# Kernel optimization log

Measured on AMD Instinct MI355X. Metric: run time of the kernel, lower is better.

Reference implementation:

```python
import jax, jax.numpy as jnp
import numpy as np

VMF_KAPPA = 30.0      # vMF concentration
THRESHOLD = 0.0       # vc_thresholds
OCC_LIKELY = 0.6      # occ_likely[0]
NUM_MIXTURES = 4
EPS_L1 = 1e-12        # torch F.normalize eps


def _l1_normalize(x, axis):
    n = jnp.sum(jnp.abs(x), axis=axis, keepdims=True)
    return x / jnp.maximum(n, EPS_L1)


def _crop_or_pad(mm, H, W):
    # center crop or zero-pad mix model spatial dims to (H, W); shapes are static
    _, _, hm, wm = mm.shape
    if hm < H:
        d1 = (H - hm) // 2
        mm = jnp.pad(mm, ((0, 0), (0, 0), (d1, H - hm - d1), (0, 0)))
    elif hm > H:
        d1 = (hm - H) // 2
        mm = mm[:, :, d1:d1 + H, :]
    if wm < W:
        d1 = (W - wm) // 2
        mm = jnp.pad(mm, ((0, 0), (0, 0), (0, 0), (d1, W - wm - d1)))
    elif wm > W:
        d1 = (wm - W) // 2
        mm = mm[:, :, :, d1:d1 + W]
    return mm


def setup_inputs() -> dict:
    key = jax.random.key(0)
    k1, k2, k3, k4 = jax.random.split(key, 4)
    B, C, H, W = 32, 512, 56, 56
    VC = 512              # number of vMF codebook vectors
    KM = 48               # num_classes(12) * num_mixtures(4)
    NCLUT = 5             # clutter models
    return {
        "vgg_feat": jax.random.normal(k1, (B, C, H, W), dtype=jnp.float32),
        "conv_weight": jax.random.normal(k2, (VC, C, 1, 1), dtype=jnp.float32),
        "mix_model": jax.random.uniform(k3, (KM, VC, H, W), dtype=jnp.float32),
        "clutter_model": jax.random.uniform(k4, (NCLUT, VC), dtype=jnp.float32),
    }


def reference(vgg_feat, conv_weight, mix_model, clutter_model):
    B, C, H, W = vgg_feat.shape
    # --- Conv1o1: cosine similarity between L2-normalized features and codebook ---
    xnorm = jnp.linalg.norm(vgg_feat, axis=1, keepdims=True)
    xnorm = xnorm + (xnorm == 0).astype(vgg_feat.dtype)  # avoid div-by-zero
    xn = vgg_feat / xnorm
    w = conv_weight[:, :, 0, 0]                           # (vc, C) 1x1 kernel
    wn = w / jnp.linalg.norm(w, axis=1, keepdims=True)
    cos = jnp.einsum('bchw,kc->bkhw', xn, wn)             # (B, vc, H, W)
    # --- vMF activation ---
    act = jnp.exp(VMF_KAPPA * cos) * (cos > THRESHOLD).astype(cos.dtype)
    # --- PointwiseInferenceLayer (vmf, use_mixture_bg=True) ---
    ck = _l1_normalize(jnp.clip(clutter_model, 0.0, 1.0), axis=1)  # (N, vc)
    bg = jnp.einsum('bkhw,nk->bnhw', act, ck)                      # (B, N, H, W)
    background = jnp.log(bg * OCC_LIKELY + 1e-10)
    background = jnp.max(background, axis=1, keepdims=True)        # (B, 1, H, W)
    background = background[:, None, None]                         # (B,1,1,1,H,W)

    mm = _l1_normalize(jnp.clip(mix_model, 0.0, 1.0), axis=1)      # (KM, vc, Hm, Wm)
    mm = _crop_or_pad(mm, H, W)
    fg = jnp.einsum('bkhw,mkhw->bmhw', act, mm)                    # (B, KM, H, W)
    foreground = jnp.log(fg * (1.0 - OCC_LIKELY) + 1e-10)
    num_classes = mm.shape[0] // NUM_MIXTURES
    foreground = foreground.reshape(B, num_classes, NUM_MIXTURES, 1, H, W)
    per_model = jnp.maximum(foreground, background).sum(axis=(-1, -2))  # (B,K,M,1)
    scores = per_model.max(axis=-1).max(axis=-1)                        # (B, K)
    mix_likeli = scores / (H * W)
    # SoftMaxTemp(2.0)
    z = jnp.exp(jnp.clip(mix_likeli * 2.0, -88.7, 88.7))
    soft = z / jnp.sum(z, axis=1, keepdims=True)
    return soft, vgg_feat, mix_likeli
```

## Files before the change

kernel.cpp:

```cpp
#include <hip/hip_runtime.h>

#define B_ 32
#define C_ 512
#define HW_ 3136
#define KF_ 512
#define KM_ 48
#define NCL_ 5

typedef __attribute__((ext_vector_type(8))) short short8;
typedef __attribute__((ext_vector_type(4))) short short4v;
typedef __attribute__((ext_vector_type(4))) float floatx4;
typedef unsigned int u32;
typedef u32 __attribute__((address_space(1))) gu32;
typedef u32 __attribute__((address_space(3))) lu32;

__device__ __forceinline__ unsigned short f2bf(float f) {
    union { float f; unsigned u; } v; v.f = f;
    unsigned r = v.u + 0x7FFFu + ((v.u >> 16) & 1u);
    return (unsigned short)(r >> 16);
}
__device__ __forceinline__ float bf2f(unsigned short u) {
    union { unsigned u; float f; } v; v.u = ((unsigned)u) << 16;
    return v.f;
}
__device__ __forceinline__ void gl2lds16(const unsigned short* g, unsigned short* l) {
    __builtin_amdgcn_global_load_lds((const gu32*)g, (lu32*)l, 16, 0, 0);
}

__global__ __launch_bounds__(64) void prep_kernel(const float* __restrict__ w,
                                                  const float* __restrict__ cl,
                                                  unsigned short* __restrict__ wn,
                                                  float* __restrict__ ck) {
    int bid = blockIdx.x, t = threadIdx.x;
    if (bid < KF_) {
        const float* row = w + (size_t)bid * C_;
        float ss = 0.f;
        float x[8];
#pragma unroll
        for (int j = 0; j < 8; ++j) { x[j] = row[t * 8 + j]; ss += x[j] * x[j]; }
        for (int m = 32; m >= 1; m >>= 1) ss += __shfl_xor(ss, m);
        float inv = 1.f / sqrtf(ss);
#pragma unroll
        for (int j = 0; j < 8; ++j) wn[(size_t)bid * C_ + t * 8 + j] = f2bf(x[j] * inv);
    } else {
        int n = bid - KF_;
        if (n >= NCL_) return;
        const float* row = cl + (size_t)n * KF_;
        float s = 0.f;
        float v[8];
#pragma unroll
        for (int j = 0; j < 8; ++j) {
            float x = row[t * 8 + j];
            x = fminf(fmaxf(x, 0.f), 1.f);
            v[j] = x; s += x;
        }
        for (int m = 32; m >= 1; m >>= 1) s += __shfl_xor(s, m);
        float inv = 1.f / fmaxf(s, 1e-12f);
#pragma unroll
        for (int j = 0; j < 8; ++j) ck[(size_t)n * KF_ + t * 8 + j] = v[j] * inv;
    }
}

__global__ __launch_bounds__(512) void xprep_kernel(const float* __restrict__ vgg,
                                                    unsigned short* __restrict__ xnt,
                                                    float* __restrict__ invn,
                                                    float* __restrict__ out_vgg,
                                                    int write_vgg) {
    int pt = blockIdx.x, b = blockIdx.y;
    int tid = threadIdx.x;
    int px = tid & 63, cq = tid >> 6;
    __shared__ __align__(16) unsigned short tile[64][512];
    __shared__ float ssp[8][64];
    const float* vcol = vgg + (size_t)b * C_ * HW_ + pt * 64 + px;
    float* ovcol = out_vgg + (size_t)b * C_ * HW_ + pt * 64 + px;

    float ss = 0.f;
#pragma unroll
    for (int j = 0; j < 16; ++j) {
        int c0 = cq * 64 + j * 4;
        float x0 = vcol[(size_t)(c0 + 0) * HW_];
        float x1 = vcol[(size_t)(c0 + 1) * HW_];
        float x2 = vcol[(size_t)(c0 + 2) * HW_];
        float x3 = vcol[(size_t)(c0 + 3) * HW_];
        ss += x0 * x0 + x1 * x1 + x2 * x2 + x3 * x3;
        short4v pk;
        pk[0] = (short)f2bf(x0); pk[1] = (short)f2bf(x1);
        pk[2] = (short)f2bf(x2); pk[3] = (short)f2bf(x3);
        *(short4v*)&tile[px][c0] = pk;
        if (write_vgg) {
            ovcol[(size_t)(c0 + 0) * HW_] = x0;
            ovcol[(size_t)(c0 + 1) * HW_] = x1;
            ovcol[(size_t)(c0 + 2) * HW_] = x2;
            ovcol[(size_t)(c0 + 3) * HW_] = x3;
        }
    }
    ssp[cq][px] = ss;
    __syncthreads();
    if (tid < 64) {
        float s = 0.f;
#pragma unroll
        for (int q = 0; q < 8; ++q) s += ssp[q][tid];
        float n = sqrtf(s);
        invn[(size_t)b * HW_ + pt * 64 + tid] = (n == 0.f) ? 1.f : 1.f / n;
    }
    __syncthreads();
    int row = tid >> 3, ch = tid & 7;
    unsigned short* orow = xnt + ((size_t)b * HW_ + pt * 64 + row) * 512;
#pragma unroll
    for (int j = 0; j < 8; ++j) {
        int c8 = (ch + 8 * j) * 8;
        *(short8*)(orow + c8) = *(const short8*)&tile[row][c8];
    }
}

__global__ __launch_bounds__(256) void gemm_act_kernel(const unsigned short* __restrict__ xnt,
                                                       const unsigned short* __restrict__ wn,
                                                       const float* __restrict__ invn,
                                                       const float* __restrict__ ck,
                                                       unsigned short* __restrict__ act,
                                                       float* __restrict__ bgacc) {
    int pt = blockIdx.x, ft = blockIdx.y;
    int tid = threadIdx.x, lane = tid & 63, w = tid >> 6;
    int wm = w & 1, wq = w >> 1;
    __shared__ __align__(16) unsigned short a_lds[128 * 64];
    __shared__ __align__(16) unsigned short b_lds[128 * 64];
    __shared__ float ck_l[NCL_ * KF_];
    __shared__ float inv_l[128];
    __shared__ float bga_l[128 * NCL_];

    for (int i = tid; i < NCL_ * KF_; i += 256) ck_l[i] = ck[i];
    if (tid < 128) inv_l[tid] = invn[(size_t)pt * 128 + tid];
    for (int i = tid; i < 128 * NCL_; i += 256) bga_l[i] = 0.f;

    const unsigned short* ga = wn + ((size_t)(ft * 128) + (tid >> 3)) * 512 + (tid & 7) * 8;
    const unsigned short* gb = xnt + ((size_t)pt * 128 + (tid >> 3)) * 512 + (tid & 7) * 8;
    unsigned short* la = a_lds + (tid >> 3) * 64 + (tid & 7) * 8;
    unsigned short* lb = b_lds + (tid >> 3) * 64 + (tid & 7) * 8;

    floatx4 acc[4][4] = {};
    for (int ks = 0; ks < 8; ++ks) {
#pragma unroll
        for (int s = 0; s < 4; ++s) {
            gl2lds16(ga + (size_t)s * 32 * 512 + ks * 64, la + s * 32 * 64);
            gl2lds16(gb + (size_t)s * 32 * 512 + ks * 64, lb + s * 32 * 64);
        }
        __syncthreads();
#pragma unroll
        for (int k2 = 0; k2 < 2; ++k2) {
            short8 af[4], bf[4];
#pragma unroll
            for (int i = 0; i < 4; ++i) {
                af[i] = *(const short8*)&a_lds[(wm * 64 + i * 16 + (lane & 15)) * 64 + k2 * 32 + (lane >> 4) * 8];
                bf[i] = *(const short8*)&b_lds[(wq * 64 + i * 16 + (lane & 15)) * 64 + k2 * 32 + (lane >> 4) * 8];
            }
#pragma unroll
            for (int mi = 0; mi < 4; ++mi)
#pragma unroll
                for (int ni = 0; ni < 4; ++ni)
                    acc[mi][ni] = __builtin_amdgcn_mfma_f32_16x16x32_bf16(af[mi], bf[ni], acc[mi][ni], 0, 0, 0);
        }
        __syncthreads();
    }

#pragma unroll
    for (int ni = 0; ni < 4; ++ni) {
        int px_l = wq * 64 + ni * 16 + (lane & 15);
        float inv = inv_l[px_l];
        size_t row_g = (size_t)pt * 128 + px_l;
        float bp[NCL_] = {0.f, 0.f, 0.f, 0.f, 0.f};
#pragma unroll
        for (int mi = 0; mi < 4; ++mi) {
            int f_g = ft * 128 + wm * 64 + mi * 16 + (lane >> 4) * 4;
            short4v pk;
            float av[4];
#pragma unroll
            for (int r = 0; r < 4; ++r) {
                float cv = acc[mi][ni][r] * inv;
                float a = cv > 0.f ? __expf(30.f * cv) : 0.f;
                av[r] = a;
                pk[r] = (short)f2bf(a);
            }
            *(short4v*)(act + row_g * 512 + f_g) = pk;
#pragma unroll
            for (int n = 0; n < NCL_; ++n)
                bp[n] += av[0] * ck_l[n * KF_ + f_g] + av[1] * ck_l[n * KF_ + f_g + 1] +
                         av[2] * ck_l[n * KF_ + f_g + 2] + av[3] * ck_l[n * KF_ + f_g + 3];
        }
#pragma unroll
        for (int n = 0; n < NCL_; ++n) {
            float v = bp[n];
            v += __shfl_xor(v, 16);
            v += __shfl_xor(v, 32);
            if ((lane >> 4) == 0) atomicAdd(&bga_l[px_l * NCL_ + n], v);
        }
    }
    __syncthreads();
    if (tid < 128) {
        size_t row_g = (size_t)pt * 128 + tid;
#pragma unroll
        for (int n = 0; n < NCL_; ++n)
            atomicAdd(&bgacc[row_g * 8 + n], bga_l[tid * NCL_ + n]);
    }
}

__global__ __launch_bounds__(512, 4) void fg_kernel(const unsigned short* __restrict__ act,
                                                    const float* __restrict__ mm,
                                                    const float* __restrict__ bgacc,
                                                    float* __restrict__ pm) {
    int p0 = blockIdx.x * 16;
    int mt = blockIdx.y;
    int tid = threadIdx.x;
    int lane = tid & 63, wid = tid >> 6;

    __shared__ __align__(16) unsigned short actl[4 * 4224];
    __shared__ __align__(16) unsigned short mml[4 * 2176];
    __shared__ float csum_s[16 * 16];
    __shared__ float pms[16 * 32];
    __shared__ float bgs[32 * 16];

    if (tid < 256) csum_s[tid] = 0.f;
    pms[tid] = 0.f;
    {
        int bb = tid >> 4, pp = tid & 15;
        const float* bga = bgacc + ((size_t)bb * HW_ + p0 + pp) * 8;
        float mx = -1e30f;
#pragma unroll
        for (int n = 0; n < NCL_; ++n) mx = fmaxf(mx, logf(bga[n] * 0.6f + 1e-10f));
        bgs[tid] = mx;
    }

    int akg = tid & 3, ap = (tid >> 2) & 15, ab0 = tid >> 6;
    int mmm = tid >> 5, mkq = (tid >> 2) & 7, mpq = tid & 3;
    const float* mbase = mm + ((size_t)(mt * 16 + mmm) * KF_ + mkq * 4) * HW_ + p0 + mpq * 4;

    const short8* fA[2];
    const short8* fB[2][2];
#pragma unroll
    for (int e = 0; e < 2; ++e) {
        int pp = wid * 2 + e;
        fA[e] = (const short8*)&mml[(lane >> 4) * 2176 + pp * 136 + (lane & 15) * 8];
#pragma unroll
        for (int bf = 0; bf < 2; ++bf)
            fB[e][bf] = (const short8*)&actl[(lane >> 4) * 4224 + pp * 264 + (bf * 16 + (lane & 15)) * 8];
    }

    floatx4 acc[2][2] = {};
    float csr[4] = {};

    short8 areg[4];
    floatx4 mreg[4];
#pragma unroll
    for (int j = 0; j < 4; ++j)
        areg[j] = *(const short8*)(act + ((size_t)(ab0 + j * 8) * HW_ + p0 + ap) * KF_ + akg * 8);
#pragma unroll
    for (int kk = 0; kk < 4; ++kk)
        mreg[kk] = *(const floatx4*)(mbase + (size_t)kk * HW_);

    for (int ch = 0; ch < 16; ++ch) {
        __syncthreads();
#pragma unroll
        for (int j = 0; j < 4; ++j)
            *(short8*)&actl[akg * 4224 + ap * 264 + (ab0 + j * 8) * 8] = areg[j];
#pragma unroll
        for (int i = 0; i < 4; ++i) {
            float c0 = fminf(fmaxf(mreg[0][i], 0.f), 1.f);
            float c1 = fminf(fmaxf(mreg[1][i], 0.f), 1.f);
            float c2 = fminf(fmaxf(mreg[2][i], 0.f), 1.f);
            float c3 = fminf(fmaxf(mreg[3][i], 0.f), 1.f);
            csr[i] += c0 + c1 + c2 + c3;
            short4v pk;
            pk[0] = (short)f2bf(c0); pk[1] = (short)f2bf(c1);
            pk[2] = (short)f2bf(c2); pk[3] = (short)f2bf(c3);
            *(short4v*)&mml[(mkq >> 1) * 2176 + (mpq * 4 + i) * 136 + mmm * 8 + (mkq & 1) * 4] = pk;
        }
        if (ch < 15) {
            int k0 = (ch + 1) * 32;
#pragma unroll
            for (int j = 0; j < 4; ++j)
                areg[j] = *(const short8*)(act + ((size_t)(ab0 + j * 8) * HW_ + p0 + ap) * KF_ + k0 + akg * 8);
#pragma unroll
            for (int kk = 0; kk < 4; ++kk)
                mreg[kk] = *(const floatx4*)(mbase + (size_t)(k0 + kk) * HW_);
        }
        __syncthreads();
#pragma unroll
        for (int e = 0; e < 2; ++e) {
            short8 af = *fA[e];
            short8 b0 = *fB[e][0];
            short8 b1 = *fB[e][1];
            acc[e][0] = __builtin_amdgcn_mfma_f32_16x16x32_bf16(af, b0, acc[e][0], 0, 0, 0);
            acc[e][1] = __builtin_amdgcn_mfma_f32_16x16x32_bf16(af, b1, acc[e][1], 0, 0, 0);
        }
    }

#pragma unroll
    for (int i = 0; i < 4; ++i)
        atomicAdd(&csum_s[mmm * 16 + mpq * 4 + i], csr[i]);
    __syncthreads();

#pragma unroll
    for (int e = 0; e < 2; ++e) {
        int pp = wid * 2 + e;
#pragma unroll
        for (int bf = 0; bf < 2; ++bf) {
            int bcol = bf * 16 + (lane & 15);
            float bgv = bgs[bcol * 16 + pp];
#pragma unroll
            for (int r = 0; r < 4; ++r) {
                int m = (lane >> 4) * 4 + r;
                float invn = 1.f / fmaxf(csum_s[m * 16 + pp], 1e-12f);
                float v = fmaxf(logf(acc[e][bf][r] * invn * 0.4f + 1e-10f), bgv);
                atomicAdd(&pms[m * 32 + bcol], v);
            }
        }
    }
    __syncthreads();
    {
        int m = tid >> 5, bcol = tid & 31;
        atomicAdd(&pm[(size_t)bcol * KM_ + mt * 16 + m], pms[m * 32 + bcol]);
    }
}

__global__ __launch_bounds__(64) void final_kernel(const float* __restrict__ pm,
                                                   float* __restrict__ out_soft,
                                                   float* __restrict__ out_ml) {
    int b = threadIdx.x;
    if (b >= B_) return;
    float ml[12];
#pragma unroll
    for (int c = 0; c < 12; ++c) {
        float s = -1e30f;
#pragma unroll
        for (int j = 0; j < 4; ++j) s = fmaxf(s, pm[(size_t)b * KM_ + c * 4 + j]);
        ml[c] = s / (float)HW_;
    }
    float z[12], zs = 0.f;
#pragma unroll
    for (int c = 0; c < 12; ++c) {
        float e = fminf(fmaxf(ml[c] * 2.f, -88.7f), 88.7f);
        z[c] = expf(e); zs += z[c];
    }
#pragma unroll
    for (int c = 0; c < 12; ++c) {
        out_soft[(size_t)b * 12 + c] = z[c] / zs;
        out_ml[(size_t)b * 12 + c] = ml[c];
    }
}

extern "C" void kernel_launch(void* const* d_in, const int* in_sizes, int n_in,
                              void* d_out, int out_size, void* d_ws, size_t ws_size,
                              hipStream_t stream) {
    const float* vgg = (const float*)d_in[0];
    const float* cw  = (const float*)d_in[1];
    const float* mmp = (const float*)d_in[2];
    const float* cl  = (const float*)d_in[3];
    float* out = (float*)d_out;
    char* ws = (char*)d_ws;

    unsigned short* wn   = (unsigned short*)(ws);
    float* ck            = (float*)(ws + 524288);
    float* invn          = (float*)(ws + 534528);
    float* pm            = (float*)(ws + 935936);
    float* bgacc         = (float*)(ws + 942080);
    unsigned short* xnt  = (unsigned short*)(ws + 4153344);
    const size_t ACT_OFF = 4153344 + 102760448;
    const size_t ACT_BYTES = (size_t)B_ * HW_ * KF_ * 2;

    int big_ws = (ws_size >= ACT_OFF + ACT_BYTES) ? 1 : 0;
    unsigned short* act = big_ws ? (unsigned short*)(ws + ACT_OFF)
                                 : (unsigned short*)(out + 384);

    hipMemsetAsync(pm, 0, (size_t)B_ * KM_ * sizeof(float), stream);
    hipMemsetAsync(bgacc, 0, (size_t)B_ * HW_ * 8 * sizeof(float), stream);
    prep_kernel<<<dim3(KF_ + NCL_), dim3(64), 0, stream>>>(cw, cl, wn, ck);
    xprep_kernel<<<dim3(49, 32), dim3(512), 0, stream>>>(vgg, xnt, invn, out + 384, big_ws);
    gemm_act_kernel<<<dim3(784, 4), dim3(256), 0, stream>>>(xnt, wn, invn, ck, act, bgacc);
    fg_kernel<<<dim3(196, 3), dim3(512), 0, stream>>>(act, mmp, bgacc, pm);
    final_kernel<<<1, 64, 0, stream>>>(pm, out, out + 384 + (size_t)B_ * C_ * HW_);
    if (!big_ws)
        hipMemcpyAsync(out + 384, vgg, (size_t)B_ * C_ * HW_ * sizeof(float),
                       hipMemcpyDeviceToDevice, stream);
}
```

Measured before the change: 496.4 us.

## Chunk act layout by K and process all 48 mixtures per fg block

The act tensor is now written in a K-chunked layout (16 chunks of 32 features, pixel-major within each chunk), so each fg block reads a contiguous 64-byte run per pixel per chunk. fg_kernel drops the 3-way mixture split in the grid and has each block compute all 48 mixtures for its 16 pixels, so act is read once from global memory instead of three times. The cost is a larger per-thread register footprint (48 prefetched mix-model floats plus 12 accumulators), more shared memory, and only 196 blocks, which may leave the GPU's compute units underfilled.

```diff
diff --git a/kernel.cpp b/kernel.cpp
--- a/kernel.cpp
+++ b/kernel.cpp
@@ -171,6 +171,8 @@
 #pragma unroll
         for (int mi = 0; mi < 4; ++mi) {
             int f_g = ft * 128 + wm * 64 + mi * 16 + (lane >> 4) * 4;
+            int chn = ft * 4 + wm * 2 + (mi >> 1);
+            int kin = (mi & 1) * 16 + (lane >> 4) * 4;
             short4v pk;
             float av[4];
 #pragma unroll
@@ -180,7 +182,7 @@
                 av[r] = a;
                 pk[r] = (short)f2bf(a);
             }
-            *(short4v*)(act + row_g * 512 + f_g) = pk;
+            *(short4v*)(act + ((size_t)chn * 100352 + row_g) * 32 + kin) = pk;
 #pragma unroll
             for (int n = 0; n < NCL_; ++n)
                 bp[n] += av[0] * ck_l[n * KF_ + f_g] + av[1] * ck_l[n * KF_ + f_g + 1] +
@@ -203,121 +205,149 @@
     }
 }
 
-__global__ __launch_bounds__(512, 4) void fg_kernel(const unsigned short* __restrict__ act,
-                                                    const float* __restrict__ mm,
-                                                    const float* __restrict__ bgacc,
-                                                    float* __restrict__ pm) {
+__global__ __launch_bounds__(512) void fg_kernel(const unsigned short* __restrict__ act,
+                                                 const float* __restrict__ mm,
+                                                 const float* __restrict__ bgacc,
+                                                 float* __restrict__ pm) {
     int p0 = blockIdx.x * 16;
-    int mt = blockIdx.y;
     int tid = threadIdx.x;
     int lane = tid & 63, wid = tid >> 6;
-
-    __shared__ __align__(16) unsigned short actl[4 * 4224];
-    __shared__ __align__(16) unsigned short mml[4 * 2176];
-    __shared__ float csum_s[16 * 16];
-    __shared__ float pms[16 * 32];
-    __shared__ float bgs[32 * 16];
-
-    if (tid < 256) csum_s[tid] = 0.f;
-    pms[tid] = 0.f;
+    int li = lane & 15, q = lane >> 4;
+
+    __shared__ __align__(16) unsigned short actl[16 * 1154];
+    __shared__ __align__(16) unsigned short mml[16 * 1730];
+    __shared__ float csum_s[768];
+    __shared__ float pms[1536];
+    __shared__ float bgs[512];
+
+    for (int i = tid; i < 768; i += 512) csum_s[i] = 0.f;
+    for (int i = tid; i < 1536; i += 512) pms[i] = 0.f;
     {
-        int bb = tid >> 4, pp = tid & 15;
-        const float* bga = bgacc + ((size_t)bb * HW_ + p0 + pp) * 8;
+        int b = tid >> 4, px = tid & 15;
+        const float* bga = bgacc + ((size_t)b * HW_ + p0 + px) * 8;
         float mx = -1e30f;
 #pragma unroll
         for (int n = 0; n < NCL_; ++n) mx = fmaxf(mx, logf(bga[n] * 0.6f + 1e-10f));
         bgs[tid] = mx;
     }
 
-    int akg = tid & 3, ap = (tid >> 2) & 15, ab0 = tid >> 6;
-    int mmm = tid >> 5, mkq = (tid >> 2) & 7, mpq = tid & 3;
-    const float* mbase = mm + ((size_t)(mt * 16 + mmm) * KF_ + mkq * 4) * HW_ + p0 + mpq * 4;
-
-    const short8* fA[2];
-    const short8* fB[2][2];
+    int sb = tid >> 4, spx = tid & 15;
+    int m1 = sb;
+    int m2 = 32 + (sb & 15);
+    int kqo = (tid >> 8) * 4;
+
+    const unsigned short* ap = act + ((size_t)sb * HW_ + p0 + spx) * 32;
+    const float* mp1 = mm + (size_t)m1 * KF_ * HW_ + p0 + spx;
+    const float* mp2 = mm + ((size_t)m2 * KF_ + kqo * 4) * HW_ + p0 + spx;
+
+    unsigned short* awr = &actl[spx * 1154 + sb * 36];
+    unsigned short* mwr1 = &mml[spx * 1730 + m1 * 36];
+    unsigned short* mwr2 = &mml[spx * 1730 + m2 * 36];
+
+    float csum1 = 0.f, csum2 = 0.f;
+    short8 areg[4];
+    float m1r[32], m2r[16];
+    floatx4 acc[2][3][2] = {};
+
+#pragma unroll
+    for (int j = 0; j < 4; ++j) areg[j] = *(const short8*)(ap + j * 8);
+#pragma unroll
+    for (int kq = 0; kq < 8; ++kq)
+#pragma unroll
+        for (int kk = 0; kk < 4; ++kk)
+            m1r[kq * 4 + kk] = mp1[(size_t)(kq * 4 + kk) * HW_];
+#pragma unroll
+    for (int jj = 0; jj < 4; ++jj)
+#pragma unroll
+        for (int kk = 0; kk < 4; ++kk)
+            m2r[jj * 4 + kk] = mp2[(size_t)(jj * 4 + kk) * HW_];
+
+#pragma unroll 1
+    for (int ch = 0; ch < 16; ++ch) {
+        __syncthreads();
+#pragma unroll
+        for (int j = 0; j < 4; ++j) *(short8*)(awr + j * 8) = areg[j];
+#pragma unroll
+        for (int kq = 0; kq < 8; ++kq) {
+            short4v pk;
+#pragma unroll
+            for (int kk = 0; kk < 4; ++kk) {
+                float x = fminf(fmaxf(m1r[kq * 4 + kk], 0.f), 1.f);
+                csum1 += x;
+                pk[kk] = (short)f2bf(x);
+            }
+            *(short4v*)(mwr1 + kq * 4) = pk;
+        }
+#pragma unroll
+        for (int jj = 0; jj < 4; ++jj) {
+            short4v pk;
+#pragma unroll
+            for (int kk = 0; kk < 4; ++kk) {
+                float x = fminf(fmaxf(m2r[jj * 4 + kk], 0.f), 1.f);
+                csum2 += x;
+                pk[kk] = (short)f2bf(x);
+            }
+            *(short4v*)(mwr2 + (kqo + jj) * 4) = pk;
+        }
+        __syncthreads();
+        if (ch < 15) {
+            ap += (size_t)100352 * 32;
+            mp1 += (size_t)32 * HW_;
+            mp2 += (size_t)32 * HW_;
+#pragma unroll
+            for (int j = 0; j < 4; ++j) areg[j] = *(const short8*)(ap + j * 8);
+#pragma unroll
+            for (int kq = 0; kq < 8; ++kq)
+#pragma unroll
+                for (int kk = 0; kk < 4; ++kk)
+                    m1r[kq * 4 + kk] = mp1[(size_t)(kq * 4 + kk) * HW_];
+#pragma unroll
+            for (int jj = 0; jj < 4; ++jj)
+#pragma unroll
+                for (int kk = 0; kk < 4; ++kk)
+                    m2r[jj * 4 + kk] = mp2[(size_t)(jj * 4 + kk) * HW_];
+        }
+#pragma unroll
+        for (int e = 0; e < 2; ++e) {
+            int pp = wid * 2 + e;
+            short8 bfr0 = *(const short8*)&actl[pp * 1154 + li * 36 + q * 8];
+            short8 bfr1 = *(const short8*)&actl[pp * 1154 + (16 + li) * 36 + q * 8];
+#pragma unroll
+            for (int mf = 0; mf < 3; ++mf) {
+                short8 af = *(const short8*)&mml[pp * 1730 + (mf * 16 + li) * 36 + q * 8];
+                acc[e][mf][0] = __builtin_amdgcn_mfma_f32_16x16x32_bf16(af, bfr0, acc[e][mf][0], 0, 0, 0);
+                acc[e][mf][1] = __builtin_amdgcn_mfma_f32_16x16x32_bf16(af, bfr1, acc[e][mf][1], 0, 0, 0);
+            }
+        }
+    }
+
+    csum_s[m1 * 16 + spx] = csum1;
+    atomicAdd(&csum_s[m2 * 16 + spx], csum2);
+    __syncthreads();
+
 #pragma unroll
     for (int e = 0; e < 2; ++e) {
         int pp = wid * 2 + e;
-        fA[e] = (const short8*)&mml[(lane >> 4) * 2176 + pp * 136 + (lane & 15) * 8];
-#pragma unroll
-        for (int bf = 0; bf < 2; ++bf)
-            fB[e][bf] = (const short8*)&actl[(lane >> 4) * 4224 + pp * 264 + (bf * 16 + (lane & 15)) * 8];
-    }
-
-    floatx4 acc[2][2] = {};
-    float csr[4] = {};
-
-    short8 areg[4];
-    floatx4 mreg[4];
-#pragma unroll
-    for (int j = 0; j < 4; ++j)
-        areg[j] = *(const short8*)(act + ((size_t)(ab0 + j * 8) * HW_ + p0 + ap) * KF_ + akg * 8);
-#pragma unroll
-    for (int kk = 0; kk < 4; ++kk)
-        mreg[kk] = *(const floatx4*)(mbase + (size_t)kk * HW_);
-
-    for (int ch = 0; ch < 16; ++ch) {
-        __syncthreads();
-#pragma unroll
-        for (int j = 0; j < 4; ++j)
-            *(short8*)&actl[akg * 4224 + ap * 264 + (ab0 + j * 8) * 8] = areg[j];
-#pragma unroll
-        for (int i = 0; i < 4; ++i) {
-            float c0 = fminf(fmaxf(mreg[0][i], 0.f), 1.f);
-            float c1 = fminf(fmaxf(mreg[1][i], 0.f), 1.f);
-            float c2 = fminf(fmaxf(mreg[2][i], 0.f), 1.f);
-            float c3 = fminf(fmaxf(mreg[3][i], 0.f), 1.f);
-            csr[i] += c0 + c1 + c2 + c3;
-            short4v pk;
-            pk[0] = (short)f2bf(c0); pk[1] = (short)f2bf(c1);
-            pk[2] = (short)f2bf(c2); pk[3] = (short)f2bf(c3);
-            *(short4v*)&mml[(mkq >> 1) * 2176 + (mpq * 4 + i) * 136 + mmm * 8 + (mkq & 1) * 4] = pk;
-        }
-        if (ch < 15) {
-            int k0 = (ch + 1) * 32;
-#pragma unroll
-            for (int j = 0; j < 4; ++j)
-                areg[j] = *(const short8*)(act + ((size_t)(ab0 + j * 8) * HW_ + p0 + ap) * KF_ + k0 + akg * 8);
-#pragma unroll
-            for (int kk = 0; kk < 4; ++kk)
-                mreg[kk] = *(const floatx4*)(mbase + (size_t)(k0 + kk) * HW_);
-        }
-        __syncthreads();
-#pragma unroll
-        for (int e = 0; e < 2; ++e) {
-            short8 af = *fA[e];
-            short8 b0 = *fB[e][0];
-            short8 b1 = *fB[e][1];
-            acc[e][0] = __builtin_amdgcn_mfma_f32_16x16x32_bf16(af, b0, acc[e][0], 0, 0, 0);
-            acc[e][1] = __builtin_amdgcn_mfma_f32_16x16x32_bf16(af, b1, acc[e][1], 0, 0, 0);
-        }
-    }
-
-#pragma unroll
-    for (int i = 0; i < 4; ++i)
-        atomicAdd(&csum_s[mmm * 16 + mpq * 4 + i], csr[i]);
+#pragma unroll
+        for (int bf = 0; bf < 2; ++bf) {
+            int b = bf * 16 + li;
+            float bgv = bgs[b * 16 + pp];
+#pragma unroll
+            for (int mf = 0; mf < 3; ++mf) {
+#pragma unroll
+                for (int r = 0; r < 4; ++r) {
+                    int m = mf * 16 + q * 4 + r;
+                    float inv = 1.f / fmaxf(csum_s[m * 16 + pp], 1e-12f);
+                    float v = fmaxf(logf(acc[e][mf][bf][r] * inv * 0.4f + 1e-10f), bgv);
+                    atomicAdd(&pms[m * 32 + b], v);
+                }
+            }
+        }
+    }
     __syncthreads();
-
-#pragma unroll
-    for (int e = 0; e < 2; ++e) {
-        int pp = wid * 2 + e;
-#pragma unroll
-        for (int bf = 0; bf < 2; ++bf) {
-            int bcol = bf * 16 + (lane & 15);
-            float bgv = bgs[bcol * 16 + pp];
-#pragma unroll
-            for (int r = 0; r < 4; ++r) {
-                int m = (lane >> 4) * 4 + r;
-                float invn = 1.f / fmaxf(csum_s[m * 16 + pp], 1e-12f);
-                float v = fmaxf(logf(acc[e][bf][r] * invn * 0.4f + 1e-10f), bgv);
-                atomicAdd(&pms[m * 32 + bcol], v);
-            }
-        }
-    }
-    __syncthreads();
-    {
-        int m = tid >> 5, bcol = tid & 31;
-        atomicAdd(&pm[(size_t)bcol * KM_ + mt * 16 + m], pms[m * 32 + bcol]);
+    for (int i = tid; i < 1536; i += 512) {
+        int m = i >> 5, b = i & 31;
+        atomicAdd(&pm[(size_t)b * KM_ + m], pms[i]);
     }
 }
 
@@ -375,7 +405,7 @@
     prep_kernel<<<dim3(KF_ + NCL_), dim3(64), 0, stream>>>(cw, cl, wn, ck);
     xprep_kernel<<<dim3(49, 32), dim3(512), 0, stream>>>(vgg, xnt, invn, out + 384, big_ws);
     gemm_act_kernel<<<dim3(784, 4), dim3(256), 0, stream>>>(xnt, wn, invn, ck, act, bgacc);
-    fg_kernel<<<dim3(196, 3), dim3(512), 0, stream>>>(act, mmp, bgacc, pm);
+    fg_kernel<<<dim3(196), dim3(512), 0, stream>>>(act, mmp, bgacc, pm);
     final_kernel<<<1, 64, 0, stream>>>(pm, out, out + 384 + (size_t)B_ * C_ * HW_);
     if (!big_ws)
         hipMemcpyAsync(out + 384, vgg, (size_t)B_ * C_ * HW_ * sizeof(float),
```

Measured after the change: 504.1 us. About the same (+1.6%).
